# Kernel tuning notes

Hardware: AMD Instinct MI355X
Metric: run time of the kernel (lower is better)

Reference implementation:

```python
import jax, jax.numpy as jnp
import numpy as np

PATCH = 16  # conv kernel size == stride


def _patch_embed(im, W, b):
    # im: (B, C, H, W) NCHW; W: (hidden, C, s, s); returns (B, h, w, hidden)
    out = jax.lax.conv_general_dilated(
        im, W, window_strides=(PATCH, PATCH), padding='VALID',
        dimension_numbers=('NCHW', 'OIHW', 'NCHW'))
    out = out + b[None, :, None, None]
    return jnp.transpose(out, (0, 2, 3, 1))  # (B, h, w, hidden)


def setup_inputs() -> dict:
    key = jax.random.key(0)
    k1, k2, k3, k4 = jax.random.split(key, 4)
    B, C, H, Wd = 64, 3, 224, 224
    hidden = 384
    x = jax.random.normal(k1, (B, C, H, Wd), dtype=jnp.float32)
    y = jax.random.normal(k2, (B, C, H, Wd), dtype=jnp.float32)
    fan_in = C * PATCH * PATCH
    bound = 1.0 / np.sqrt(fan_in)
    W = jax.random.uniform(k3, (hidden, C, PATCH, PATCH), dtype=jnp.float32,
                           minval=-bound, maxval=bound)
    b = jax.random.uniform(k4, (hidden,), dtype=jnp.float32,
                           minval=-bound, maxval=bound)
    return {'x': x, 'y': y, 'W': W, 'b': b}


def reference(x, y, W, b):
    B = x.shape[0]
    xp = _patch_embed(x, W, b)  # (B, h, w, C)
    yp = _patch_embed(y, W, b)  # (B, h, w, C)
    h, w = xp.shape[1], xp.shape[2]
    logp = jax.nn.log_softmax(xp, axis=-1)          # (B, h, w, C)
    q = jax.lax.stop_gradient(jax.nn.softmax(yp, axis=-1))  # detached targets
    # CE[i, j] = mean over (h, w) of -(q_j * logp_i).sum(-1)
    # Faithful factorization of the (B, B, h, w, C) broadcast in the original.
    CE = -jnp.einsum('ihwc,jhwc->ij', logp, q) / (h * w)  # (B, B)
    close = jnp.trace(CE) / B
    far = (CE.sum() - jnp.trace(CE)) / (B * B - B)
    return close / far
```

## Files before the change

### kernel.cpp

```cpp
#include <hip/hip_runtime.h>

#define HID   384
#define K_PE  768
#define IMGST 150528
#define NCOLS 75264
#define XPHALF 9633792

typedef unsigned short ushort_t;
using f32x4  = __attribute__((ext_vector_type(4))) float;
using short8 = __attribute__((ext_vector_type(8))) short;

__device__ __forceinline__ unsigned bfpack(float lo, float hi) {
    union { float f; unsigned u; } a, b; a.f = lo; b.f = hi;
    unsigned ra = (a.u + 0x7fffu + ((a.u >> 16) & 1u)) >> 16;
    unsigned rb = (b.u + 0x7fffu + ((b.u >> 16) & 1u)) & 0xffff0000u;
    return ra | rb;
}

__device__ __forceinline__ void gl_lds16(const void* g, void* l) {
    __builtin_amdgcn_global_load_lds(
        (const __attribute__((address_space(1))) unsigned*)g,
        (__attribute__((address_space(3))) unsigned*)l, 16, 0, 0);
}

__global__ __launch_bounds__(256) void pe_prep(
    const float* __restrict__ x, const float* __restrict__ y,
    const float* __restrict__ W, ushort_t* __restrict__ Wfrag,
    ushort_t* __restrict__ Xp, float* __restrict__ scal,
    float* __restrict__ Lsum, float* __restrict__ Qsum) {
    const int t = blockIdx.x * 256 + threadIdx.x;
    if (t < 4) scal[t] = 0.f;
    if (t < NCOLS / 4) {
        ((float4*)Lsum)[t] = float4{0.f, 0.f, 0.f, 0.f};
        ((float4*)Qsum)[t] = float4{0.f, 0.f, 0.f, 0.f};
    }
    if (t < 36864) {
        const int n  = t / 96;
        const int ko = t % 96;
        const float4 a = *(const float4*)(W + (size_t)n * K_PE + ko * 8);
        const float4 b = *(const float4*)(W + (size_t)n * K_PE + ko * 8 + 4);
        uint4 pk;
        pk.x = bfpack(a.x, a.y); pk.y = bfpack(a.z, a.w);
        pk.z = bfpack(b.x, b.y); pk.w = bfpack(b.z, b.w);
        const int nt   = n >> 4;
        const int kc   = ko >> 2;
        const int lane = (ko & 3) * 16 + (n & 15);
        ((uint4*)Wfrag)[(nt * 24 + kc) * 64 + lane] = pk;
    }
    const int o = t % 96;
    int rest    = t / 96;
    const int i = rest & 63;
    rest >>= 6;
    const int p = rest % 196;
    const int z = rest / 196;
    const int c    = o >> 5;
    const int di   = (o >> 1) & 15;
    const int half = o & 1;
    const int pi   = p / 14;
    const int pj   = p - pi * 14;
    const float* src = (z ? y : x) +
        ((size_t)(i * 3 + c) * 224 + pi * 16 + di) * 224 + pj * 16 + half * 8;
    float4 f0 = *(const float4*)src;
    float4 f1 = *(const float4*)(src + 4);
    uint4 pk;
    pk.x = bfpack(f0.x, f0.y); pk.y = bfpack(f0.z, f0.w);
    pk.z = bfpack(f1.x, f1.y); pk.w = bfpack(f1.z, f1.w);
    const int op = (o & ~7) | ((o & 7) ^ (i & 7));
    ((uint4*)Xp)[(size_t)z * 1204224 + (size_t)(p * 64 + i) * 96 + op] = pk;
}

__global__ __launch_bounds__(256, 3) void pe_gemm(
    const ushort_t* __restrict__ Xp, const ushort_t* __restrict__ Wfrag,
    const float* __restrict__ bias, float* __restrict__ scal,
    float* __restrict__ Lsum, float* __restrict__ Qsum) {
    const int p  = blockIdx.x;
    const int ig = blockIdx.y;

    __shared__ __align__(16) ushort_t As[2][16 * 768];
    __shared__ float Smx[4][16], Ssx[4][16], Smy[4][16], Ssy[4][16];
    __shared__ float sT[4];

    const int tid  = threadIdx.x;
    const int wave = tid >> 6;
    const int lane = tid & 63;
    const int lm   = lane & 15;
    const int lq   = lane >> 4;
    const int wn   = wave * 96;

    {
        const ushort_t* xs = Xp + (size_t)(p * 64 + ig * 16) * 768;
        const ushort_t* ys = xs + XPHALF;
#pragma unroll
        for (int c6 = 0; c6 < 6; ++c6) {
            const int ch = wave * 6 + c6;
            gl_lds16(xs + (size_t)ch * 512 + lane * 8, &As[0][ch * 512]);
            gl_lds16(ys + (size_t)ch * 512 + lane * 8, &As[1][ch * 512]);
        }
    }

    const ushort_t* bbase = Wfrag + (size_t)lane * 8;
    f32x4 accx[6] = {};
    f32x4 accy[6] = {};

    __syncthreads();

#pragma unroll
    for (int kbi = 0; kbi < 12; ++kbi) {
#pragma unroll
        for (int ks = 0; ks < 2; ++ks) {
            short8 bfr[6];
#pragma unroll
            for (int ni = 0; ni < 6; ++ni)
                bfr[ni] = *(const short8*)(bbase +
                          (size_t)(((wave * 6 + ni) * 24 + kbi * 2 + ks) * 64) * 8);
            const int aoff = lm * 768 +
                             (kbi * 8 + ((ks * 4 + lq) ^ (lm & 7))) * 8;
            short8 afx = *(const short8*)&As[0][aoff];
            short8 afy = *(const short8*)&As[1][aoff];
#pragma unroll
            for (int ni = 0; ni < 6; ++ni) {
                accx[ni] = __builtin_amdgcn_mfma_f32_16x16x32_bf16(
                    afx, bfr[ni], accx[ni], 0, 0, 0);
                accy[ni] = __builtin_amdgcn_mfma_f32_16x16x32_bf16(
                    afy, bfr[ni], accy[ni], 0, 0, 0);
            }
        }
    }

#pragma unroll
    for (int ni = 0; ni < 6; ++ni) {
        const float bv = bias[wn + ni * 16 + lm];
#pragma unroll
        for (int r = 0; r < 4; ++r) {
            accx[ni][r] += bv;
            accy[ni][r] += bv;
        }
    }

    float mx[4], my_[4];
#pragma unroll
    for (int r = 0; r < 4; ++r) {
        float a = accx[0][r], b = accy[0][r];
#pragma unroll
        for (int ni = 1; ni < 6; ++ni) {
            a = fmaxf(a, accx[ni][r]);
            b = fmaxf(b, accy[ni][r]);
        }
        mx[r] = a; my_[r] = b;
    }
#pragma unroll
    for (int off = 1; off < 16; off <<= 1)
#pragma unroll
        for (int r = 0; r < 4; ++r) {
            mx[r]  = fmaxf(mx[r],  __shfl_xor(mx[r],  off));
            my_[r] = fmaxf(my_[r], __shfl_xor(my_[r], off));
        }
    if (lm == 0)
#pragma unroll
        for (int r = 0; r < 4; ++r) {
            Smx[wave][lq * 4 + r] = mx[r];
            Smy[wave][lq * 4 + r] = my_[r];
        }
    __syncthreads();
#pragma unroll
    for (int r = 0; r < 4; ++r) {
        const int row = lq * 4 + r;
        mx[r]  = fmaxf(fmaxf(Smx[0][row], Smx[1][row]),
                       fmaxf(Smx[2][row], Smx[3][row]));
        my_[r] = fmaxf(fmaxf(Smy[0][row], Smy[1][row]),
                       fmaxf(Smy[2][row], Smy[3][row]));
    }

    float sx[4], sy[4];
#pragma unroll
    for (int r = 0; r < 4; ++r) {
        float a = 0.f, b = 0.f;
#pragma unroll
        for (int ni = 0; ni < 6; ++ni) {
            a += __expf(accx[ni][r] - mx[r]);
            b += __expf(accy[ni][r] - my_[r]);
        }
        sx[r] = a; sy[r] = b;
    }
#pragma unroll
    for (int off = 1; off < 16; off <<= 1)
#pragma unroll
        for (int r = 0; r < 4; ++r) {
            sx[r] += __shfl_xor(sx[r], off);
            sy[r] += __shfl_xor(sy[r], off);
        }
    if (lm == 0)
#pragma unroll
        for (int r = 0; r < 4; ++r) {
            Ssx[wave][lq * 4 + r] = sx[r];
            Ssy[wave][lq * 4 + r] = sy[r];
        }
    __syncthreads();
#pragma unroll
    for (int r = 0; r < 4; ++r) {
        const int row = lq * 4 + r;
        const float ssx = Ssx[0][row] + Ssx[1][row] + Ssx[2][row] + Ssx[3][row];
        const float ssy = Ssy[0][row] + Ssy[1][row] + Ssy[2][row] + Ssy[3][row];
        sx[r] = mx[r] + __logf(ssx);
        sy[r] = 1.f / ssy;
    }

    float T = 0.f;
    float cL[6], cQ[6];
#pragma unroll
    for (int ni = 0; ni < 6; ++ni) { cL[ni] = 0.f; cQ[ni] = 0.f; }
#pragma unroll
    for (int r = 0; r < 4; ++r) {
        const float sh  = sx[r];
        const float m   = my_[r];
        const float inv = sy[r];
#pragma unroll
        for (int ni = 0; ni < 6; ++ni) {
            const float lp = accx[ni][r] - sh;
            const float qv = __expf(accy[ni][r] - m) * inv;
            T += lp * qv;
            cL[ni] += lp;
            cQ[ni] += qv;
        }
    }
#pragma unroll
    for (int ni = 0; ni < 6; ++ni) {
        cL[ni] += __shfl_xor(cL[ni], 16); cL[ni] += __shfl_xor(cL[ni], 32);
        cQ[ni] += __shfl_xor(cQ[ni], 16); cQ[ni] += __shfl_xor(cQ[ni], 32);
    }
    if (lq == 0)
#pragma unroll
        for (int ni = 0; ni < 6; ++ni) {
            const int col = p * HID + wn + ni * 16 + lm;
            atomicAdd(&Lsum[col], cL[ni]);
            atomicAdd(&Qsum[col], cQ[ni]);
        }
#pragma unroll
    for (int off = 32; off > 0; off >>= 1) T += __shfl_xor(T, off);
    if (lane == 0) sT[wave] = T;
    __syncthreads();
    if (tid == 0)
        atomicAdd(&scal[0], sT[0] + sT[1] + sT[2] + sT[3]);
}

__global__ __launch_bounds__(256) void final_dot(const float* __restrict__ Lsum,
                                                 const float* __restrict__ Qsum,
                                                 float* __restrict__ scal,
                                                 float* __restrict__ out) {
    const int idx = blockIdx.x * 256 + threadIdx.x;
    float s = 0.f;
    if (idx < NCOLS / 4) {
        float4 a = ((const float4*)Lsum)[idx];
        float4 b = ((const float4*)Qsum)[idx];
        s = a.x * b.x + a.y * b.y + a.z * b.z + a.w * b.w;
    }
#pragma unroll
    for (int off = 32; off > 0; off >>= 1) s += __shfl_xor(s, off);
    __shared__ float sS[4];
    __shared__ int lastflag;
    if ((threadIdx.x & 63) == 0) sS[threadIdx.x >> 6] = s;
    __syncthreads();
    if (threadIdx.x == 0) {
        atomicAdd(&scal[1], sS[0] + sS[1] + sS[2] + sS[3]);
        __threadfence();
        int old = atomicAdd((int*)&scal[3], 1);
        lastflag = (old == (int)gridDim.x - 1);
    }
    __syncthreads();
    if (lastflag && threadIdx.x == 0) {
        float S = atomicAdd(&scal[1], 0.f);
        float T = atomicAdd(&scal[0], 0.f);
        out[0] = 63.f * T / (S - T);
    }
}

extern "C" void kernel_launch(void* const* d_in, const int* in_sizes, int n_in,
                              void* d_out, int out_size, void* d_ws, size_t ws_size,
                              hipStream_t stream) {
    const float* x = (const float*)d_in[0];
    const float* y = (const float*)d_in[1];
    const float* W = (const float*)d_in[2];
    const float* b = (const float*)d_in[3];
    float* out = (float*)d_out;

    float*    scal  = (float*)d_ws;
    float*    Lsum  = scal + 16;
    float*    Qsum  = Lsum + NCOLS;
    ushort_t* Wfrag = (ushort_t*)(Qsum + NCOLS);
    ushort_t* Xp    = Wfrag + 294912;

    pe_prep<<<9408, 256, 0, stream>>>(x, y, W, Wfrag, Xp, scal, Lsum, Qsum);
    pe_gemm<<<dim3(196, 4), 256, 0, stream>>>(Xp, Wfrag, b, scal, Lsum, Qsum);
    final_dot<<<74, 256, 0, stream>>>(Lsum, Qsum, scal, out);
}
```

Before: 164.6 us.

## Software-pipeline B/A fragment loads in patch GEMM and add nontemporal hints

Restructures the MFMA loop in the patch-embedding GEMM into a flattened 24-step loop that loads the next step's weight and LDS fragments before issuing the current step's MFMAs. The intent is to hide global and LDS load latency behind matrix ops. It also marks the prep kernel's bf16 patch stores and the GEMM's global-to-LDS loads as nontemporal, to reduce cache pollution from streamed data. Double-buffered fragments raise register pressure under the 3-blocks-per-SM launch bound, and since the loop was already fully unrolled the compiler may have been scheduling these loads similarly.

```diff
diff --git a/kernel.cpp b/kernel.cpp
--- a/kernel.cpp
+++ b/kernel.cpp
@@ -9,6 +9,7 @@
 typedef unsigned short ushort_t;
 using f32x4  = __attribute__((ext_vector_type(4))) float;
 using short8 = __attribute__((ext_vector_type(8))) short;
+using uint4v = __attribute__((ext_vector_type(4))) unsigned int;
 
 __device__ __forceinline__ unsigned bfpack(float lo, float hi) {
     union { float f; unsigned u; } a, b; a.f = lo; b.f = hi;
@@ -17,10 +18,10 @@
     return ra | rb;
 }
 
-__device__ __forceinline__ void gl_lds16(const void* g, void* l) {
+__device__ __forceinline__ void gl_lds16_nt(const void* g, void* l) {
     __builtin_amdgcn_global_load_lds(
         (const __attribute__((address_space(1))) unsigned*)g,
-        (__attribute__((address_space(3))) unsigned*)l, 16, 0, 0);
+        (__attribute__((address_space(3))) unsigned*)l, 16, 0, 2);
 }
 
 __global__ __launch_bounds__(256) void pe_prep(
@@ -62,11 +63,12 @@
         ((size_t)(i * 3 + c) * 224 + pi * 16 + di) * 224 + pj * 16 + half * 8;
     float4 f0 = *(const float4*)src;
     float4 f1 = *(const float4*)(src + 4);
-    uint4 pk;
+    uint4v pk;
     pk.x = bfpack(f0.x, f0.y); pk.y = bfpack(f0.z, f0.w);
     pk.z = bfpack(f1.x, f1.y); pk.w = bfpack(f1.z, f1.w);
     const int op = (o & ~7) | ((o & 7) ^ (i & 7));
-    ((uint4*)Xp)[(size_t)z * 1204224 + (size_t)(p * 64 + i) * 96 + op] = pk;
+    __builtin_nontemporal_store(pk,
+        (uint4v*)Xp + (size_t)z * 1204224 + (size_t)(p * 64 + i) * 96 + op);
 }
 
 __global__ __launch_bounds__(256, 3) void pe_gemm(
@@ -93,39 +95,53 @@
 #pragma unroll
         for (int c6 = 0; c6 < 6; ++c6) {
             const int ch = wave * 6 + c6;
-            gl_lds16(xs + (size_t)ch * 512 + lane * 8, &As[0][ch * 512]);
-            gl_lds16(ys + (size_t)ch * 512 + lane * 8, &As[1][ch * 512]);
+            gl_lds16_nt(xs + (size_t)ch * 512 + lane * 8, &As[0][ch * 512]);
+            gl_lds16_nt(ys + (size_t)ch * 512 + lane * 8, &As[1][ch * 512]);
         }
     }
 
     const ushort_t* bbase = Wfrag + (size_t)lane * 8;
+#define BPTR(STEP, NI) ((const short8*)(bbase + \
+        (size_t)(((wave * 6 + (NI)) * 24 + (STEP)) * 64) * 8))
+#define AOFF(STEP) (lm * 768 + (((STEP) >> 1) * 8 + \
+        (((((STEP) & 1) * 4) + lq) ^ (lm & 7))) * 8)
+
     f32x4 accx[6] = {};
     f32x4 accy[6] = {};
 
-    __syncthreads();
-
-#pragma unroll
-    for (int kbi = 0; kbi < 12; ++kbi) {
-#pragma unroll
-        for (int ks = 0; ks < 2; ++ks) {
-            short8 bfr[6];
-#pragma unroll
-            for (int ni = 0; ni < 6; ++ni)
-                bfr[ni] = *(const short8*)(bbase +
-                          (size_t)(((wave * 6 + ni) * 24 + kbi * 2 + ks) * 64) * 8);
-            const int aoff = lm * 768 +
-                             (kbi * 8 + ((ks * 4 + lq) ^ (lm & 7))) * 8;
-            short8 afx = *(const short8*)&As[0][aoff];
-            short8 afy = *(const short8*)&As[1][aoff];
-#pragma unroll
-            for (int ni = 0; ni < 6; ++ni) {
-                accx[ni] = __builtin_amdgcn_mfma_f32_16x16x32_bf16(
-                    afx, bfr[ni], accx[ni], 0, 0, 0);
-                accy[ni] = __builtin_amdgcn_mfma_f32_16x16x32_bf16(
-                    afy, bfr[ni], accy[ni], 0, 0, 0);
-            }
-        }
-    }
+    short8 bcur[6], bnxt[6];
+#pragma unroll
+    for (int ni = 0; ni < 6; ++ni) bcur[ni] = *BPTR(0, ni);
+
+    __syncthreads();
+
+    short8 axc = *(const short8*)&As[0][AOFF(0)];
+    short8 ayc = *(const short8*)&As[1][AOFF(0)];
+
+#pragma unroll
+    for (int step = 0; step < 24; ++step) {
+        short8 axn, ayn;
+        if (step < 23) {
+#pragma unroll
+            for (int ni = 0; ni < 6; ++ni) bnxt[ni] = *BPTR(step + 1, ni);
+            axn = *(const short8*)&As[0][AOFF(step + 1)];
+            ayn = *(const short8*)&As[1][AOFF(step + 1)];
+        }
+#pragma unroll
+        for (int ni = 0; ni < 6; ++ni) {
+            accx[ni] = __builtin_amdgcn_mfma_f32_16x16x32_bf16(
+                axc, bcur[ni], accx[ni], 0, 0, 0);
+            accy[ni] = __builtin_amdgcn_mfma_f32_16x16x32_bf16(
+                ayc, bcur[ni], accy[ni], 0, 0, 0);
+        }
+        if (step < 23) {
+#pragma unroll
+            for (int ni = 0; ni < 6; ++ni) bcur[ni] = bnxt[ni];
+            axc = axn; ayc = ayn;
+        }
+    }
+#undef BPTR
+#undef AOFF
 
 #pragma unroll
     for (int ni = 0; ni < 6; ++ni) {
```

After: 162.3 us. About the same (-1.4%).
